# Optimization experiments

Hardware: AMD Instinct MI355X
Metric: run time of the kernel (lower is better)

Reference implementation:

```python
import jax, jax.numpy as jnp
import numpy as np


def setup_inputs() -> dict:
    key = jax.random.key(0)
    ks = jax.random.split(key, 7)
    B, I, H = 8192, 1024, 1024
    x = jax.random.normal(ks[0], (B, I), dtype=jnp.float32)
    h_prev = jax.random.normal(ks[1], (B, H), dtype=jnp.float32)
    C_prev = jax.random.normal(ks[2], (B, H), dtype=jnp.float32)
    W_f = jax.random.normal(ks[3], (I + H, H), dtype=jnp.float32) * 0.01
    W_i = jax.random.normal(ks[4], (I + H, H), dtype=jnp.float32) * 0.01
    W_C = jax.random.normal(ks[5], (I + H, H), dtype=jnp.float32) * 0.01
    W_o = jax.random.normal(ks[6], (I + H, H), dtype=jnp.float32) * 0.01
    b = jnp.zeros((H,), dtype=jnp.float32)
    return {"x": x, "h_prev": h_prev, "C_prev": C_prev,
            "W_f": W_f, "b_f": b, "W_i": W_i, "b_i": b,
            "W_C": W_C, "b_C": b, "W_o": W_o, "b_o": b}


def reference(x, h_prev, C_prev, W_f, b_f, W_i, b_i, W_C, b_C, W_o, b_o):
    combined = jnp.concatenate([x, h_prev], axis=1)  # [B, I+H]
    # Fuse the four gate GEMMs into one [B, I+H] x [I+H, 4H] matmul.
    W = jnp.concatenate([W_f, W_i, W_o, W_C], axis=1)  # [I+H, 4H]
    b = jnp.concatenate([b_f, b_i, b_o, b_C], axis=0)  # [4H]
    gates = combined @ W + b                            # [B, 4H]
    H = C_prev.shape[1]
    f_t = jax.nn.sigmoid(gates[:, 0:H])
    i_t = jax.nn.sigmoid(gates[:, H:2 * H])
    o_t = jax.nn.sigmoid(gates[:, 2 * H:3 * H])
    C_tilda = jnp.tanh(gates[:, 3 * H:4 * H])
    C_t = f_t * C_prev + i_t * C_tilda
    h_t = o_t * jnp.tanh(C_t)
    return (h_t, C_t)
```

## Files before the change

### kernel.cpp

```cpp
#include <hip/hip_runtime.h>
#include <hip/hip_bf16.h>

#define B_SZ 8192
#define IH   2048
#define H_SZ 1024
#define BMR  128
#define BK   32
#define NKT  (IH / BK)
#define BUFB 24576
#define WOF2 8192

typedef __attribute__((ext_vector_type(8))) short  short8;
typedef __attribute__((ext_vector_type(4))) float  floatx4;

static __device__ __forceinline__ ushort f2bf(float f) {
  union { float f; unsigned u; } v; v.f = f;
  unsigned u = v.u;
  u += 0x7fffu + ((u >> 16) & 1u);
  return (ushort)(u >> 16);
}
static __device__ __forceinline__ float sigmoidf_(float x) {
  return 1.0f / (1.0f + __expf(-x));
}
static __device__ __forceinline__ float tanhf_(float x) {
  float ax = fabsf(x);
  float e = __expf(-2.0f * ax);
  float t = (1.0f - e) / (1.0f + e);
  return copysignf(t, x);
}
static __device__ __forceinline__ void gload_lds16(const void* gsrc, void* ldst) {
  __builtin_amdgcn_global_load_lds(
      (__attribute__((address_space(1))) const void*)gsrc,
      (__attribute__((address_space(3))) void*)ldst, 16, 0, 0);
}

__global__ __launch_bounds__(256) void convert_w_kernel(
    const float* __restrict__ Wf, const float* __restrict__ Wi,
    const float* __restrict__ Wo, const float* __restrict__ Wc,
    ushort* __restrict__ Wt) {
  __shared__ float tile[64][65];
  const int g  = blockIdx.z;
  const float* W = (g == 0) ? Wf : (g == 1) ? Wi : (g == 2) ? Wo : Wc;
  const int n0 = blockIdx.x * 64;
  const int k0 = blockIdx.y * 64;
  const int tid = threadIdx.x;
#pragma unroll
  for (int i = 0; i < 4; ++i) {
    int c = i * 256 + tid;
    int r = c >> 4, c4 = c & 15;
    float4 v = *(const float4*)(W + (size_t)(k0 + r) * H_SZ + n0 + c4 * 4);
    tile[r][c4 * 4 + 0] = v.x;
    tile[r][c4 * 4 + 1] = v.y;
    tile[r][c4 * 4 + 2] = v.z;
    tile[r][c4 * 4 + 3] = v.w;
  }
  __syncthreads();
  const int n  = tid >> 2;
  const int kc = (tid & 3) * 16;
  ushort o[16] __attribute__((aligned(16)));
#pragma unroll
  for (int e = 0; e < 16; ++e) o[e] = f2bf(tile[kc + e][n]);
  ushort* dst = Wt + ((size_t)g * H_SZ + n0 + n) * IH + k0 + kc;
  *(uint4*)(dst)     = *(uint4*)&o[0];
  *(uint4*)(dst + 8) = *(uint4*)&o[8];
}

__global__ __launch_bounds__(256) void convert_a_kernel(
    const float* __restrict__ x, const float* __restrict__ hp,
    ushort* __restrict__ Abf) {
  size_t idx = ((size_t)blockIdx.x * 256 + threadIdx.x) * 8;
  size_t row = idx >> 11;
  size_t col = idx & 2047;
  const float* src = (col < 1024) ? (x  + row * 1024 + col)
                                  : (hp + row * 1024 + (col - 1024));
  float4 v0 = *(const float4*)(src);
  float4 v1 = *(const float4*)(src + 4);
  ushort o[8] __attribute__((aligned(16)));
  o[0] = f2bf(v0.x); o[1] = f2bf(v0.y); o[2] = f2bf(v0.z); o[3] = f2bf(v0.w);
  o[4] = f2bf(v1.x); o[5] = f2bf(v1.y); o[6] = f2bf(v1.z); o[7] = f2bf(v1.w);
  *(uint4*)(Abf + idx) = *(uint4*)&o[0];
}

__global__ __launch_bounds__(256, 2) void lstm_fused_kernel(
    const float* __restrict__ Cp, const ushort* __restrict__ Wt,
    const ushort* __restrict__ Abf,
    const float* __restrict__ bf_, const float* __restrict__ bi_,
    const float* __restrict__ bo_, const float* __restrict__ bc_,
    float* __restrict__ out) {
  __shared__ char lds[2 * BUFB];

  const int bid = blockIdx.x;
  const int wg  = (bid & 7) * 128 + (bid >> 3);
  const int b0  = (wg >> 4) * BMR;
  const int n0g = (wg & 15) * 64;

  const int tid = threadIdx.x;
  const int ln  = tid & 63;
  const int wv  = tid >> 6;
  const int wm  = wv >> 1, wn = wv & 1;

  floatx4 acc[4][8];
#pragma unroll
  for (int m = 0; m < 4; ++m)
#pragma unroll
    for (int j = 0; j < 8; ++j) acc[m][j] = {0.f, 0.f, 0.f, 0.f};

  const int q  = ((ln & 15) >> 1) & 3;
  const int sx = ((ln >> 4) ^ q) << 4;
  const int aB = (wm * 64 + (ln & 15)) * 64 + sx;
  const int bB = WOF2 + (wn * 32 + (ln & 15)) * 64 + sx;

  const unsigned kg  = ((unsigned)(tid & 3)) ^ ((unsigned)(tid >> 3) & 3);
  const char* AbfB = (const char*)Abf;
  const char* WtB  = (const char*)Wt;
  unsigned aoff[2], woff[4];
#pragma unroll
  for (int i = 0; i < 2; ++i)
    aoff[i] = (unsigned)(b0 + i * 64 + (tid >> 2)) * 4096u + kg * 16u;
#pragma unroll
  for (int i = 0; i < 4; ++i)
    woff[i] = (unsigned)(i * 1024 + n0g + (tid >> 2)) * 4096u + kg * 16u;
  const int dstw = wv * 1024;

#define SAB(db, ktb)                                                          \
  do {                                                                        \
    gload_lds16(AbfB + (aoff[0] + (unsigned)(ktb)), lds + (db) + dstw);       \
    gload_lds16(AbfB + (aoff[1] + (unsigned)(ktb)), lds + (db) + 4096 + dstw);\
    gload_lds16(WtB  + (woff[0] + (unsigned)(ktb)), lds + (db) + WOF2 + dstw);\
    gload_lds16(WtB  + (woff[1] + (unsigned)(ktb)), lds + (db) + WOF2 + 4096 + dstw);\
    gload_lds16(WtB  + (woff[2] + (unsigned)(ktb)), lds + (db) + WOF2 + 8192 + dstw);\
    gload_lds16(WtB  + (woff[3] + (unsigned)(ktb)), lds + (db) + WOF2 + 12288 + dstw);\
  } while (0)

  short8 aF[4];
  short8 bF[8];
#define RD_A(db, mf)  (aF[mf] = *(const short8*)(lds + (db) + aB + (mf) * 1024))
#define RD_B(db, j)   (bF[j]  = *(const short8*)(lds + (db) + bB +            \
                                 ((j) >> 1) * 4096 + ((j) & 1) * 1024))
#define MFALL()                                                               \
  do {                                                                        \
    __builtin_amdgcn_s_setprio(1);                                            \
    _Pragma("unroll")                                                         \
    for (int mf_ = 0; mf_ < 4; ++mf_)                                         \
      _Pragma("unroll")                                                       \
      for (int j_ = 0; j_ < 8; ++j_)                                          \
        acc[mf_][j_] = __builtin_amdgcn_mfma_f32_16x16x32_bf16(               \
            aF[mf_], bF[j_], acc[mf_][j_], 0, 0, 0);                          \
    __builtin_amdgcn_s_setprio(0);                                            \
  } while (0)
#define BAR   __builtin_amdgcn_s_barrier()
#define VMC0  asm volatile("s_waitcnt vmcnt(0)" ::: "memory")

#define KTILE(db, nb, ktn)                                                    \
  do {                                                                        \
    SAB(nb, ((ktn) & 63) * 64);                                               \
    RD_A(db, 0); RD_A(db, 1); RD_A(db, 2); RD_A(db, 3);                       \
    RD_B(db, 0); RD_B(db, 1); RD_B(db, 2); RD_B(db, 3);                       \
    RD_B(db, 4); RD_B(db, 5); RD_B(db, 6); RD_B(db, 7);                       \
    MFALL();                                                                  \
    VMC0; BAR;                                                                \
  } while (0)

  SAB(0, 0);
  VMC0; BAR;

#pragma unroll 1
  for (int it = 0; it < NKT / 2; ++it) {
    KTILE(0,    BUFB, 2 * it + 1);
    KTILE(BUFB, 0,    2 * it + 2);
  }

  const int colq = ln & 15;
  const int rq   = ln >> 4;
  float* outh = out;
  float* outC = out + (size_t)B_SZ * H_SZ;
#pragma unroll
  for (int mf = 0; mf < 4; ++mf) {
#pragma unroll
    for (int ns = 0; ns < 2; ++ns) {
      int n = n0g + wn * 32 + ns * 16 + colq;
      float vbf = bf_[n], vbi = bi_[n], vbo = bo_[n], vbc = bc_[n];
#pragma unroll
      for (int r = 0; r < 4; ++r) {
        int row = b0 + wm * 64 + mf * 16 + rq * 4 + r;
        float fg = sigmoidf_(acc[mf][0 + ns][r] + vbf);
        float ig = sigmoidf_(acc[mf][2 + ns][r] + vbi);
        float og = sigmoidf_(acc[mf][4 + ns][r] + vbo);
        float cg = tanhf_  (acc[mf][6 + ns][r] + vbc);
        float cp = Cp[(size_t)row * H_SZ + n];
        float Ct = fg * cp + ig * cg;
        float ht = og * tanhf_(Ct);
        outh[(size_t)row * H_SZ + n] = ht;
        outC[(size_t)row * H_SZ + n] = Ct;
      }
    }
  }
#undef SAB
#undef RD_A
#undef RD_B
#undef MFALL
#undef BAR
#undef VMC0
#undef KTILE
}

extern "C" void kernel_launch(void* const* d_in, const int* in_sizes, int n_in,
                              void* d_out, int out_size, void* d_ws, size_t ws_size,
                              hipStream_t stream) {
  const float* x  = (const float*)d_in[0];
  const float* hp = (const float*)d_in[1];
  const float* Cp = (const float*)d_in[2];
  const float* Wf = (const float*)d_in[3];
  const float* bf = (const float*)d_in[4];
  const float* Wi = (const float*)d_in[5];
  const float* bi = (const float*)d_in[6];
  const float* Wc = (const float*)d_in[7];
  const float* bc = (const float*)d_in[8];
  const float* Wo = (const float*)d_in[9];
  const float* bo = (const float*)d_in[10];

  ushort* Wt  = (ushort*)d_ws;
  ushort* Abf = (ushort*)((char*)d_ws + (16u << 20));

  dim3 gridT(16, 32, 4);
  convert_w_kernel<<<gridT, 256, 0, stream>>>(Wf, Wi, Wo, Wc, Wt);
  convert_a_kernel<<<8192, 256, 0, stream>>>(x, hp, Abf);

  lstm_fused_kernel<<<1024, 256, 0, stream>>>(Cp, Wt, Abf,
                                              bf, bi, bo, bc, (float*)d_out);
}
```

Baseline: 172.8 us.

## Double block rows to 256 and software-pipeline LDS fragment reads into registers

Each workgroup now has 512 threads, or 8 waves, and covers 256 batch rows instead of 128, with larger double-buffered LDS stages. This halves the number of workgroups and doubles reuse of each staged weight tile. The main loop now double-buffers MFMA operand fragments in registers. The next k-tile's LDS reads and the global-to-LDS prefetch are issued before the current tile's MFMAs, so LDS latency overlaps with compute. The extra fragment registers plus the 128-register accumulator under a 512x2 launch bound raise register pressure and could cause spills or lower occupancy.

```diff
diff --git a/kernel.cpp b/kernel.cpp
--- a/kernel.cpp
+++ b/kernel.cpp
@@ -4,11 +4,11 @@
 #define B_SZ 8192
 #define IH   2048
 #define H_SZ 1024
-#define BMR  128
+#define BM   256
 #define BK   32
 #define NKT  (IH / BK)
-#define BUFB 24576
-#define WOF2 8192
+#define DB2  32768
+#define WOF  16384
 
 typedef __attribute__((ext_vector_type(8))) short  short8;
 typedef __attribute__((ext_vector_type(4))) float  floatx4;
@@ -81,17 +81,17 @@
   *(uint4*)(Abf + idx) = *(uint4*)&o[0];
 }
 
-__global__ __launch_bounds__(256, 2) void lstm_fused_kernel(
+__global__ __launch_bounds__(512, 2) void lstm_fused_kernel(
     const float* __restrict__ Cp, const ushort* __restrict__ Wt,
     const ushort* __restrict__ Abf,
     const float* __restrict__ bf_, const float* __restrict__ bi_,
     const float* __restrict__ bo_, const float* __restrict__ bc_,
     float* __restrict__ out) {
-  __shared__ char lds[2 * BUFB];
+  __shared__ char lds[2 * DB2];
 
   const int bid = blockIdx.x;
-  const int wg  = (bid & 7) * 128 + (bid >> 3);
-  const int b0  = (wg >> 4) * BMR;
+  const int wg  = (bid & 7) * 64 + (bid >> 3);
+  const int b0  = (wg >> 4) * BM;
   const int n0g = (wg & 15) * 64;
 
   const int tid = threadIdx.x;
@@ -108,36 +108,42 @@
   const int q  = ((ln & 15) >> 1) & 3;
   const int sx = ((ln >> 4) ^ q) << 4;
   const int aB = (wm * 64 + (ln & 15)) * 64 + sx;
-  const int bB = WOF2 + (wn * 32 + (ln & 15)) * 64 + sx;
-
-  const unsigned kg  = ((unsigned)(tid & 3)) ^ ((unsigned)(tid >> 3) & 3);
+  const int bB = WOF + (wn * 32 + (ln & 15)) * 64 + sx;
+
+  const unsigned kg = ((unsigned)(tid & 3)) ^ ((unsigned)(tid >> 3) & 3);
   const char* AbfB = (const char*)Abf;
   const char* WtB  = (const char*)Wt;
-  unsigned aoff[2], woff[4];
-#pragma unroll
-  for (int i = 0; i < 2; ++i)
-    aoff[i] = (unsigned)(b0 + i * 64 + (tid >> 2)) * 4096u + kg * 16u;
-#pragma unroll
-  for (int i = 0; i < 4; ++i)
-    woff[i] = (unsigned)(i * 1024 + n0g + (tid >> 2)) * 4096u + kg * 16u;
-  const int dstw = wv * 1024;
-
-#define SAB(db, ktb)                                                          \
+  unsigned aoff[2], woff[2];
+#pragma unroll
+  for (int i = 0; i < 2; ++i) {
+    int row = i * 128 + (tid >> 2);
+    aoff[i] = (unsigned)(b0 + row) * 4096u + kg * 16u;
+    int gate = row >> 6, nloc = row & 63;
+    woff[i] = (unsigned)(gate * 1024 + n0g + nloc) * 4096u + kg * 16u;
+  }
+  const int dst0 = wv * 1024;
+
+#define STAGE(db, ktb)                                                        \
   do {                                                                        \
-    gload_lds16(AbfB + (aoff[0] + (unsigned)(ktb)), lds + (db) + dstw);       \
-    gload_lds16(AbfB + (aoff[1] + (unsigned)(ktb)), lds + (db) + 4096 + dstw);\
-    gload_lds16(WtB  + (woff[0] + (unsigned)(ktb)), lds + (db) + WOF2 + dstw);\
-    gload_lds16(WtB  + (woff[1] + (unsigned)(ktb)), lds + (db) + WOF2 + 4096 + dstw);\
-    gload_lds16(WtB  + (woff[2] + (unsigned)(ktb)), lds + (db) + WOF2 + 8192 + dstw);\
-    gload_lds16(WtB  + (woff[3] + (unsigned)(ktb)), lds + (db) + WOF2 + 12288 + dstw);\
+    gload_lds16(AbfB + (aoff[0] + (unsigned)(ktb)), lds + (db) + dst0);       \
+    gload_lds16(AbfB + (aoff[1] + (unsigned)(ktb)), lds + (db) + 8192 + dst0);\
+    gload_lds16(WtB  + (woff[0] + (unsigned)(ktb)), lds + (db) + WOF + dst0); \
+    gload_lds16(WtB  + (woff[1] + (unsigned)(ktb)), lds + (db) + WOF + 8192 + dst0);\
   } while (0)
 
-  short8 aF[4];
-  short8 bF[8];
-#define RD_A(db, mf)  (aF[mf] = *(const short8*)(lds + (db) + aB + (mf) * 1024))
-#define RD_B(db, j)   (bF[j]  = *(const short8*)(lds + (db) + bB +            \
-                                 ((j) >> 1) * 4096 + ((j) & 1) * 1024))
-#define MFALL()                                                               \
+  short8 aFA[4], bFA[8];
+  short8 aFB[4], bFB[8];
+#define RDSET(AF, BF, db)                                                     \
+  do {                                                                        \
+    _Pragma("unroll")                                                         \
+    for (int mf_ = 0; mf_ < 4; ++mf_)                                         \
+      AF[mf_] = *(const short8*)(lds + (db) + aB + mf_ * 1024);               \
+    _Pragma("unroll")                                                         \
+    for (int j_ = 0; j_ < 8; ++j_)                                            \
+      BF[j_] = *(const short8*)(lds + (db) + bB + (j_ >> 1) * 4096 +          \
+                                (j_ & 1) * 1024);                             \
+  } while (0)
+#define MFALL(AF, BF)                                                         \
   do {                                                                        \
     __builtin_amdgcn_s_setprio(1);                                            \
     _Pragma("unroll")                                                         \
@@ -145,29 +151,35 @@
       _Pragma("unroll")                                                       \
       for (int j_ = 0; j_ < 8; ++j_)                                          \
         acc[mf_][j_] = __builtin_amdgcn_mfma_f32_16x16x32_bf16(               \
-            aF[mf_], bF[j_], acc[mf_][j_], 0, 0, 0);                          \
+            AF[mf_], BF[j_], acc[mf_][j_], 0, 0, 0);                          \
     __builtin_amdgcn_s_setprio(0);                                            \
   } while (0)
-#define BAR   __builtin_amdgcn_s_barrier()
-#define VMC0  asm volatile("s_waitcnt vmcnt(0)" ::: "memory")
-
-#define KTILE(db, nb, ktn)                                                    \
-  do {                                                                        \
-    SAB(nb, ((ktn) & 63) * 64);                                               \
-    RD_A(db, 0); RD_A(db, 1); RD_A(db, 2); RD_A(db, 3);                       \
-    RD_B(db, 0); RD_B(db, 1); RD_B(db, 2); RD_B(db, 3);                       \
-    RD_B(db, 4); RD_B(db, 5); RD_B(db, 6); RD_B(db, 7);                       \
-    MFALL();                                                                  \
-    VMC0; BAR;                                                                \
-  } while (0)
-
-  SAB(0, 0);
+#define BAR    __builtin_amdgcn_s_barrier()
+#define LGKM0  asm volatile("s_waitcnt lgkmcnt(0)" ::: "memory")
+#define VMC0   asm volatile("s_waitcnt vmcnt(0)" ::: "memory")
+
+  STAGE(0, 0);
+  STAGE(DB2, 64);
   VMC0; BAR;
+  RDSET(aFA, bFA, 0);
+  LGKM0; BAR;
 
 #pragma unroll 1
   for (int it = 0; it < NKT / 2; ++it) {
-    KTILE(0,    BUFB, 2 * it + 1);
-    KTILE(BUFB, 0,    2 * it + 2);
+    {
+      const int ktb = (((2 * it + 2) & 63)) * 64;
+      RDSET(aFB, bFB, DB2);
+      STAGE(0, ktb);
+      MFALL(aFA, bFA);
+      LGKM0; VMC0; BAR;
+    }
+    {
+      const int ktb = (((2 * it + 3) & 63)) * 64;
+      RDSET(aFA, bFA, 0);
+      STAGE(DB2, ktb);
+      MFALL(aFB, bFB);
+      LGKM0; VMC0; BAR;
+    }
   }
 
   const int colq = ln & 15;
@@ -195,13 +207,12 @@
       }
     }
   }
-#undef SAB
-#undef RD_A
-#undef RD_B
+#undef STAGE
+#undef RDSET
 #undef MFALL
 #undef BAR
+#undef LGKM0
 #undef VMC0
-#undef KTILE
 }
 
 extern "C" void kernel_launch(void* const* d_in, const int* in_sizes, int n_in,
@@ -226,6 +237,6 @@
   convert_w_kernel<<<gridT, 256, 0, stream>>>(Wf, Wi, Wo, Wc, Wt);
   convert_a_kernel<<<8192, 256, 0, stream>>>(x, hp, Abf);
 
-  lstm_fused_kernel<<<1024, 256, 0, stream>>>(Cp, Wt, Abf,
-                                              bf, bi, bo, bc, (float*)d_out);
-}
+  lstm_fused_kernel<<<512, 512, 0, stream>>>(Cp, Wt, Abf,
+                                             bf, bi, bo, bc, (float*)d_out);
+}
```

Result: faster. 163.8 us (-5.2%).
